# Kernel tuning notes

Hardware: AMD Instinct MI355X
Metric: run time of the kernel (lower is better)

The kernel has to match this reference:

```python
import jax, jax.numpy as jnp
import numpy as np

N_BALLS, BALL, DIM, HEADS = 16, 512, 256, 8
DH = DIM // HEADS            # 32
WIN = BALL // 16             # sliding window = 32
CBS = BALL // 16             # compress block size = 32
CST = BALL // 32             # compress stride = 16
FBS = BALL // 16             # fine (selection) block size = 32
NCB = (BALL - CBS) // CST + 1  # 31 compressed blocks
NFB = BALL // FBS              # 16 fine blocks
NB = BALL // WIN               # 16 sliding blocks
SCALE = DH ** -0.5

# ---- static index maps / masks (numpy, baked at trace time) ----
_qi = np.arange(BALL)
WIDX = np.arange(NCB)[:, None] * CST + np.arange(CBS)[None, :]          # (NCB, CBS)
_blk_end = np.arange(NCB) * CST + CBS - 1
CMASK = np.concatenate([np.ones((BALL, 1), bool), _qi[:, None] >= _blk_end[None, :]], axis=1)  # (m, NCB+1), col0 = mem kv
OVERLAP = np.zeros((NCB, NFB), np.float32)  # fraction of compressed block j overlapping fine block f
for _j in range(NCB):
    _a, _b = _j * CST, _j * CST + CBS
    for _f in range(NFB):
        _fa, _fb = _f * FBS, (_f + 1) * FBS
        OVERLAP[_j, _f] = max(0, min(_b, _fb) - max(_a, _fa)) / CBS
SELMASK = np.arange(NFB)[None, :] < (_qi // FBS)[:, None]   # only strictly-past fine blocks selectable
HAS_SEL = (_qi // FBS) > 0
OWN_TRI = (_qi % FBS)[:, None] >= np.arange(FBS)[None, :]   # causal mask inside own fine block
_qq = np.arange(WIN)[None, :, None]
_kk = np.arange(2 * WIN)[None, None, :]
_bb = np.arange(NB)[:, None, None]
SWMASK = (_kk > _qq) & (_kk <= _qq + WIN) & ((_bb > 0) | (_kk >= WIN))
NEG = -jnp.inf


def _rot(x, tpos):
    # interleaved rotary over full head dim; x: (n,H,m,DH)
    d2 = DH // 2
    inv = 1.0 / (10000.0 ** (jnp.arange(d2, dtype=jnp.float32) / d2))
    ang = tpos[:, None] * inv[None, :]
    cos, sin = jnp.cos(ang), jnp.sin(ang)
    x1, x2 = x[..., 0::2], x[..., 1::2]
    return jnp.stack((x1 * cos - x2 * sin, x1 * sin + x2 * cos), axis=-1).reshape(x.shape)


def _gmlp(xw, w1, w2):
    # per-head grouped MLP compressing each window: (n,H,NCB,CBS,DH) -> (n,H,NCB,DH)
    f = xw.reshape(xw.shape[0], HEADS, NCB, CBS * DH)
    h = jax.nn.relu(jnp.einsum('nhbi,hio->nhbo', f, w1))
    return jnp.einsum('nhbi,hio->nhbo', h, w2)


def _forward(x, pos, Wpe, bpe, rms_w, Wqkv, kpos, vpos, kw1, kw2, vw1, vw2, mem_ck, mem_cv, Wg, Wo):
    n, m = N_BALLS, BALL
    # relative position embedding w.r.t. ball center (eq. 9)
    pb = pos.reshape(n, m, -1)
    rel = pb - pb.mean(axis=1, keepdims=True)
    hx = x.reshape(n, m, DIM) + rel @ Wpe + bpe
    # RMSNorm
    hn = hx * jax.lax.rsqrt(jnp.mean(hx * hx, axis=-1, keepdims=True) + 1e-6) * rms_w
    q, k, v = jnp.split(hn @ Wqkv, 3, axis=-1)
    heads = lambda t: t.reshape(n, m, HEADS, DH).transpose(0, 2, 1, 3)
    q, k, v = heads(q), heads(k), heads(v)
    tpos = jnp.arange(m, dtype=jnp.float32)
    rq, rk = _rot(q, tpos), _rot(k, tpos)

    # ---- compressed branch (non-rotated q/k, intra-block pos emb, 1 learned mem kv) ----
    kw = k[:, :, WIDX] + kpos[None, :, None]        # (n,H,NCB,CBS,DH)
    vw = v[:, :, WIDX] + vpos[None, :, None]
    ck = _gmlp(kw, kw1, kw2)
    cv = _gmlp(vw, vw1, vw2)
    ckf = jnp.concatenate([jnp.broadcast_to(mem_ck[None], (n, HEADS, 1, DH)), ck], axis=2)
    cvf = jnp.concatenate([jnp.broadcast_to(mem_cv[None], (n, HEADS, 1, DH)), cv], axis=2)
    csim = jnp.einsum('nhid,nhjd->nhij', q, ckf) * SCALE
    cattn = jax.nn.softmax(jnp.where(CMASK[None, None], csim, NEG), axis=-1)
    c_out = jnp.einsum('nhij,nhjd->nhid', cattn, cvf)

    # ---- fine selection: importance from compressed attn probs -> top-1 past fine block ----
    imp = jnp.einsum('nhij,jf->nhif', cattn[..., 1:], jnp.asarray(OVERLAP))  # (n,H,m,NFB)
    sel = jnp.argmax(jnp.where(SELMASK[None, None], imp, NEG), axis=-1)     # (n,H,m)
    kb = rk.reshape(n, HEADS, NFB, FBS, DH)
    vb = v.reshape(n, HEADS, NFB, FBS, DH)
    qb = rq.reshape(n, HEADS, NFB, FBS, DH)
    own_s = (jnp.einsum('nhfqd,nhfkd->nhfqk', qb, kb) * SCALE).reshape(n, HEADS, m, FBS)
    fk = jnp.take_along_axis(kb, sel[..., None, None], axis=2)  # (n,H,m,FBS,DH) gather
    fv = jnp.take_along_axis(vb, sel[..., None, None], axis=2)
    sel_s = jnp.einsum('nhid,nhikd->nhik', rq, fk) * SCALE
    scores = jnp.concatenate([jnp.where(OWN_TRI[None, None], own_s, NEG),
                              jnp.where(HAS_SEL[None, None, :, None], sel_s, NEG)], axis=-1)
    fattn = jax.nn.softmax(scores, axis=-1)
    f_out = (jnp.einsum('nhfqk,nhfkd->nhfqd', fattn[..., :FBS].reshape(n, HEADS, NFB, FBS, FBS), vb).reshape(n, HEADS, m, DH)
             + jnp.einsum('nhik,nhikd->nhid', fattn[..., FBS:], fv))

    # ---- sliding window branch (causal local attention, look-back 1 block) ----
    qw = rq.reshape(n, HEADS, NB, WIN, DH)
    kwb = rk.reshape(n, HEADS, NB, WIN, DH)
    vwb = v.reshape(n, HEADS, NB, WIN, DH)
    pad = ((0, 0), (0, 0), (1, 0), (0, 0), (0, 0))
    K2 = jnp.concatenate([jnp.pad(kwb, pad)[:, :, :NB], kwb], axis=3)
    V2 = jnp.concatenate([jnp.pad(vwb, pad)[:, :, :NB], vwb], axis=3)
    s_sw = jnp.einsum('nhbqd,nhbkd->nhbqk', qw, K2) * SCALE
    sattn = jax.nn.softmax(jnp.where(SWMASK[None, None], s_sw, NEG), axis=-1)
    sw_out = jnp.einsum('nhbqk,nhbkd->nhbqd', sattn, V2).reshape(n, HEADS, m, DH)

    # ---- sigmoid-gated combine of the 3 strategies, merge heads, out proj ----
    gates = jax.nn.sigmoid(hn @ Wg).reshape(n, m, HEADS, 3).transpose(0, 2, 1, 3)  # (n,H,m,3)
    o = c_out * gates[..., 0:1] + f_out * gates[..., 1:2] + sw_out * gates[..., 2:3]
    o = o.transpose(0, 2, 1, 3).reshape(n, m, DIM)
    return (o @ Wo).reshape(n * m, DIM)


def setup_inputs() -> dict:
    key = jax.random.key(0)
    ks = jax.random.split(key, 16)
    s = 0.02
    N = N_BALLS * BALL
    return dict(
        x=jax.random.normal(ks[0], (N, DIM), jnp.float32),
        pos=jax.random.normal(ks[1], (N, 3), jnp.float32),
        Wpe=s * jax.random.normal(ks[2], (3, DIM), jnp.float32),
        bpe=jnp.zeros((DIM,), jnp.float32),
        rms_w=jnp.ones((DIM,), jnp.float32),
        Wqkv=s * jax.random.normal(ks[3], (DIM, 3 * DIM), jnp.float32),
        kpos=s * jax.random.normal(ks[4], (HEADS, CBS, DH), jnp.float32),
        vpos=s * jax.random.normal(ks[5], (HEADS, CBS, DH), jnp.float32),
        kw1=s * jax.random.normal(ks[6], (HEADS, CBS * DH, CBS * DH), jnp.float32),
        kw2=s * jax.random.normal(ks[7], (HEADS, CBS * DH, DH), jnp.float32),
        vw1=s * jax.random.normal(ks[8], (HEADS, CBS * DH, CBS * DH), jnp.float32),
        vw2=s * jax.random.normal(ks[9], (HEADS, CBS * DH, DH), jnp.float32),
        mem_ck=s * jax.random.normal(ks[10], (HEADS, 1, DH), jnp.float32),
        mem_cv=s * jax.random.normal(ks[11], (HEADS, 1, DH), jnp.float32),
        Wg=s * jax.random.normal(ks[12], (DIM, 3 * HEADS), jnp.float32),
        Wo=s * jax.random.normal(ks[13], (DIM, DIM), jnp.float32),
    )


def reference(x, pos, Wpe, bpe, rms_w, Wqkv, kpos, vpos, kw1, kw2, vw1, vw2, mem_ck, mem_cv, Wg, Wo):
    return _forward(x, pos, Wpe, bpe, rms_w, Wqkv, kpos, vpos, kw1, kw2, vw1, vw2, mem_ck, mem_cv, Wg, Wo)
```

## Files before the change

### kernel.cpp

```cpp
#include <hip/hip_runtime.h>
#include <hip/hip_bf16.h>
#include <math.h>

#define SCALE_ 0.17677669529663687f

__global__ __launch_bounds__(256) void d_rope(float* __restrict__ rope) {
  int i = blockIdx.x * 256 + threadIdx.x;
  int t = i >> 4, j = i & 15;
  float inv = powf(10000.f, -(float)j / 16.f);
  float ang = (float)t * inv;
  rope[2 * i]     = cosf(ang);
  rope[2 * i + 1] = sinf(ang);
}

__global__ __launch_bounds__(256) void k_pm(const float* __restrict__ pos,
                                            float* __restrict__ pm) {
  __shared__ float ps[1536];
  int ball = blockIdx.x;
  for (int i = threadIdx.x; i < 1536; i += 256) ps[i] = pos[(size_t)ball * 1536 + i];
  __syncthreads();
  if (threadIdx.x < 3) {
    int c = threadIdx.x;
    float s = 0.f;
    for (int t = 0; t < 512; ++t) s += ps[t * 3 + c];
    pm[ball * 3 + c] = s * (1.f / 512.f);
  }
}

__global__ __launch_bounds__(256) void k_hn(const float* __restrict__ x,
                                            const float* __restrict__ pos,
                                            const float* __restrict__ pm,
                                            const float* __restrict__ Wpe,
                                            const float* __restrict__ bpe,
                                            const float* __restrict__ rmsw,
                                            float* __restrict__ hn) {
  __shared__ float hx[32][257];
  __shared__ float rr[32][3];
  __shared__ float invs[32];
  int tb = blockIdx.x * 32;
  if (threadIdx.x < 96) {
    int tok = threadIdx.x / 3, c = threadIdx.x % 3;
    rr[tok][c] = pos[(size_t)(tb + tok) * 3 + c] - pm[((tb + tok) >> 9) * 3 + c];
  }
  __syncthreads();
  for (int i = threadIdx.x; i < 8192; i += 256) {
    int tok = i >> 8, d = i & 255;
    float h = x[(size_t)(tb + tok) * 256 + d] + rr[tok][0] * Wpe[d] + rr[tok][1] * Wpe[256 + d]
            + rr[tok][2] * Wpe[512 + d] + bpe[d];
    hx[tok][d] = h;
  }
  __syncthreads();
  if (threadIdx.x < 32) {
    int tok = threadIdx.x;
    float ss = 0.f;
    for (int d = 0; d < 256; ++d) { float h = hx[tok][d]; ss += h * h; }
    invs[tok] = 1.f / sqrtf(ss * (1.f / 256.f) + 1e-6f);
  }
  __syncthreads();
  for (int i = threadIdx.x; i < 8192; i += 256) {
    int tok = i >> 8, d = i & 255;
    hn[(size_t)(tb + tok) * 256 + d] = hx[tok][d] * invs[tok] * rmsw[d];
  }
}

__global__ __launch_bounds__(256) void k_qkv(const float* __restrict__ A,
                                             const float* __restrict__ B,
                                             const float* __restrict__ rope,
                                             float* __restrict__ qo,
                                             float* __restrict__ ko,
                                             float* __restrict__ vo,
                                             float* __restrict__ rqo,
                                             float* __restrict__ rko) {
  __shared__ float As[32][66];
  __shared__ __align__(16) float Bs[32][68];
  const int m0 = blockIdx.x * 64;
  const int n0 = blockIdx.y * 64;
  const int tid = threadIdx.x;
  const int tx = tid & 15, ty = tid >> 4;
  float acc[4][4] = {};
  for (int k0 = 0; k0 < 256; k0 += 32) {
#pragma unroll
    for (int i = 0; i < 8; ++i) {
      int li = tid + i * 256;
      int mm = li >> 5, c = li & 31;
      As[c][mm] = A[(size_t)(m0 + mm) * 256 + k0 + c];
    }
#pragma unroll
    for (int i = 0; i < 8; ++i) {
      int li = tid + i * 256;
      int r = li >> 6, c = li & 63;
      Bs[r][c] = B[(size_t)(k0 + r) * 768 + n0 + c];
    }
    __syncthreads();
#pragma unroll
    for (int kk = 0; kk < 32; ++kk) {
      float2 a0 = *reinterpret_cast<const float2*>(&As[kk][ty * 4]);
      float2 a1 = *reinterpret_cast<const float2*>(&As[kk][ty * 4 + 2]);
      float4 b4 = *reinterpret_cast<const float4*>(&Bs[kk][tx * 4]);
      float a[4] = {a0.x, a0.y, a1.x, a1.y};
      float b[4] = {b4.x, b4.y, b4.z, b4.w};
#pragma unroll
      for (int i = 0; i < 4; ++i)
#pragma unroll
        for (int j = 0; j < 4; ++j) acc[i][j] += a[i] * b[j];
    }
    __syncthreads();
  }
#pragma unroll
  for (int i = 0; i < 4; ++i) {
    int row = m0 + ty * 4 + i;
    int nb = row >> 9, t = row & 511;
#pragma unroll
    for (int j = 0; j < 4; j += 2) {
      int col = n0 + tx * 4 + j;
      int which = col >> 8, cj = col & 255;
      int h = cj >> 5, d = cj & 31;
      float v1 = acc[i][j], v2 = acc[i][j + 1];
      size_t base = ((size_t)(nb * 8 + h) * 512 + t) * 32 + d;
      if (which == 0) {
        qo[base] = v1; qo[base + 1] = v2;
        int p = d >> 1;
        float cc = rope[(t * 16 + p) * 2], ss = rope[(t * 16 + p) * 2 + 1];
        rqo[base] = v1 * cc - v2 * ss; rqo[base + 1] = v1 * ss + v2 * cc;
      } else if (which == 1) {
        ko[base] = v1; ko[base + 1] = v2;
        int p = d >> 1;
        float cc = rope[(t * 16 + p) * 2], ss = rope[(t * 16 + p) * 2 + 1];
        rko[base] = v1 * cc - v2 * ss; rko[base + 1] = v1 * ss + v2 * cc;
      } else {
        vo[base] = v1; vo[base + 1] = v2;
      }
    }
  }
}

__global__ __launch_bounds__(256) void d_gates(const float* __restrict__ hn,
                                               const float* __restrict__ Wg,
                                               float* __restrict__ gates) {
  int gid = blockIdx.x * 256 + threadIdx.x;
  int tok = gid / 24, j = gid % 24;
  const float* hr = hn + (size_t)tok * 256;
  float s = 0.f;
  for (int d = 0; d < 256; ++d) s += hr[d] * Wg[d * 24 + j];
  gates[gid] = 1.f / (1.f + expf(-s));
}

__global__ __launch_bounds__(256) void k_gmlp1(const float* __restrict__ kv,
                                               const float* __restrict__ posw,
                                               const float* __restrict__ w1,
                                               float* __restrict__ hb) {
  __shared__ float As[32][66];
  __shared__ __align__(16) float Bs[32][68];
  const int bid = blockIdx.x;
  const int xcd = bid & 7;
  const int idx = bid >> 3;
  const int mt  = idx & 7;
  const int nh  = xcd * 16 + (idx >> 3);
  const int n0 = (nh & 15) * 64;
  const int h  = nh >> 4;
  const int m0 = mt * 64;
  const int tid = threadIdx.x;
  const int tx = tid & 15, ty = tid >> 4;
  float acc[4][4] = {};
  for (int k0 = 0; k0 < 1024; k0 += 32) {
#pragma unroll
    for (int i = 0; i < 8; ++i) {
      int li = tid + i * 256;
      int mm = li >> 5, c = li & 31;
      int row = m0 + mm;
      float vv = 0.f;
      if (row < 496) {
        int nb = row / 31, bb = row % 31;
        vv = kv[((size_t)(nb * 8 + h) * 512 + bb * 16) * 32 + k0 + c] + posw[h * 1024 + k0 + c];
      }
      As[c][mm] = vv;
    }
#pragma unroll
    for (int i = 0; i < 8; ++i) {
      int li = tid + i * 256;
      int r = li >> 6, c = li & 63;
      Bs[r][c] = w1[(size_t)h * 1048576 + (size_t)(k0 + r) * 1024 + n0 + c];
    }
    __syncthreads();
#pragma unroll
    for (int kk = 0; kk < 32; ++kk) {
      float2 a0 = *reinterpret_cast<const float2*>(&As[kk][ty * 4]);
      float2 a1 = *reinterpret_cast<const float2*>(&As[kk][ty * 4 + 2]);
      float4 b4 = *reinterpret_cast<const float4*>(&Bs[kk][tx * 4]);
      float a[4] = {a0.x, a0.y, a1.x, a1.y};
      float b[4] = {b4.x, b4.y, b4.z, b4.w};
#pragma unroll
      for (int i = 0; i < 4; ++i)
#pragma unroll
        for (int j = 0; j < 4; ++j) acc[i][j] += a[i] * b[j];
    }
    __syncthreads();
  }
#pragma unroll
  for (int i = 0; i < 4; ++i) {
    int row = m0 + ty * 4 + i;
    if (row < 496) {
#pragma unroll
      for (int j = 0; j < 4; ++j)
        hb[((size_t)h * 496 + row) * 1024 + n0 + tx * 4 + j] = fmaxf(acc[i][j], 0.f);
    }
  }
}

__global__ __launch_bounds__(256) void d_g2(const float* __restrict__ hh,
                                            const float* __restrict__ w2,
                                            float* __restrict__ outp) {
  int gid = blockIdx.x * 256 + threadIdx.x;
  int o = gid & 31;
  int rem = gid >> 5;
  int h = rem / 496, row = rem % 496;
  int nb = row / 31, bb = row % 31;
  const float* hr = hh + (size_t)rem * 1024;
  const float* w2p = w2 + (size_t)h * 32768 + o;
  float s = 0.f;
  for (int i = 0; i < 1024; ++i) s += hr[i] * w2p[(size_t)i * 32];
  outp[((size_t)(nb * 8 + h) * 31 + bb) * 32 + o] = s;
}

__global__ __launch_bounds__(256) void d_cattn(const float* __restrict__ q,
                                               const float* __restrict__ ck,
                                               const float* __restrict__ cv,
                                               const float* __restrict__ mem_ck,
                                               const float* __restrict__ mem_cv,
                                               const float* __restrict__ gates,
                                               float* __restrict__ obuf,
                                               int* __restrict__ sel) {
  int gid = blockIdx.x * 256 + threadIdx.x;
  int nh = gid >> 9, t = gid & 511;
  int h = nh & 7, ball = nh >> 3;
  const float* qp = q + (size_t)gid * 32;
  float sc[32];
  float mx = -INFINITY;
#pragma unroll
  for (int j = 0; j < 32; ++j) {
    float s = -INFINITY;
    bool valid = (j == 0) || (t >= (j - 1) * 16 + 31);
    if (valid) {
      const float* kp = (j == 0) ? (mem_ck + h * 32)
                                 : (ck + ((size_t)nh * 31 + (j - 1)) * 32);
      s = 0.f;
      for (int d = 0; d < 32; ++d) s += qp[d] * kp[d];
      s *= SCALE_;
    }
    sc[j] = s;
    mx = fmaxf(mx, s);
  }
  float e[32];
  float den = 0.f;
#pragma unroll
  for (int j = 0; j < 32; ++j) { e[j] = expf(sc[j] - mx); den += e[j]; }
  float num[32];
#pragma unroll
  for (int d = 0; d < 32; ++d) num[d] = 0.f;
#pragma unroll
  for (int j = 0; j < 32; ++j) {
    const float* vp = (j == 0) ? (mem_cv + h * 32)
                               : (cv + ((size_t)nh * 31 + (j - 1)) * 32);
    float p = e[j];
    for (int d = 0; d < 32; ++d) num[d] += p * vp[d];
  }
  float inv = 1.f / den;
  float g0 = gates[(size_t)(ball * 512 + t) * 24 + h * 3];
  float* op = obuf + (size_t)(ball * 512 + t) * 256 + h * 32;
  for (int d = 0; d < 32; ++d) op[d] = num[d] * inv * g0;

  int s_idx = 0;
  if (t >= 32) {
    int fn = t >> 5;
    float best = -INFINITY;
    for (int f = 0; f < fn; ++f) {
      float im = 0.f;
#pragma unroll
      for (int j = 0; j < 31; ++j) {
        int a = j * 16, b2 = a + 32, fa = f * 32, fb = fa + 32;
        int lo = a > fa ? a : fa;
        int hi = b2 < fb ? b2 : fb;
        if (hi > lo) im += e[j + 1] * (float)(hi - lo) * (1.f / 32.f);
      }
      if (im > best) { best = im; s_idx = f; }
    }
  }
  sel[gid] = s_idx;
}

__global__ __launch_bounds__(256) void k_fattn(const float* __restrict__ rq,
                                               const float* __restrict__ rk,
                                               const float* __restrict__ v,
                                               const int* __restrict__ sel,
                                               const float* __restrict__ gates,
                                               float* __restrict__ obuf) {
  int f0 = blockIdx.x, h = blockIdx.y, nb = blockIdx.z;
  int nh = nb * 8 + h;
  __shared__ float rqs[32][33], rks[32][33], vs[32][33];
  for (int i = threadIdx.x; i < 1024; i += 256) {
    int r = i >> 5, d = i & 31;
    size_t base = ((size_t)nh * 512 + f0 * 32 + r) * 32 + d;
    rqs[r][d] = rq[base];
    rks[r][d] = rk[base];
    vs[r][d]  = v[base];
  }
  __syncthreads();
  int qi = threadIdx.x >> 3, l = threadIdx.x & 7;
  int t = f0 * 32 + qi;
  int sb = sel[(size_t)nh * 512 + t];
  bool hs = (t >= 32);
  float p[8];
  float mx = -INFINITY;
#pragma unroll
  for (int kk2 = 0; kk2 < 8; ++kk2) {
    int kk = l * 8 + kk2;
    float s = -INFINITY;
    if (kk < 32) {
      if (qi >= kk) {
        s = 0.f;
#pragma unroll
        for (int d = 0; d < 32; ++d) s += rqs[qi][d] * rks[kk][d];
        s *= SCALE_;
      }
    } else if (hs) {
      const float* kp = rk + ((size_t)nh * 512 + sb * 32 + (kk - 32)) * 32;
      s = 0.f;
#pragma unroll
      for (int d = 0; d < 32; ++d) s += rqs[qi][d] * kp[d];
      s *= SCALE_;
    }
    p[kk2] = s;
    mx = fmaxf(mx, s);
  }
#pragma unroll
  for (int off = 4; off; off >>= 1) mx = fmaxf(mx, __shfl_xor(mx, off, 8));
  float sum = 0.f;
#pragma unroll
  for (int kk2 = 0; kk2 < 8; ++kk2) { p[kk2] = expf(p[kk2] - mx); sum += p[kk2]; }
#pragma unroll
  for (int off = 4; off; off >>= 1) sum += __shfl_xor(sum, off, 8);
  float inv = 1.f / sum;
  float acc[32];
#pragma unroll
  for (int d = 0; d < 32; ++d) acc[d] = 0.f;
#pragma unroll
  for (int kk2 = 0; kk2 < 8; ++kk2) {
    int kk = l * 8 + kk2;
    float pw = p[kk2] * inv;
    if (kk < 32) {
#pragma unroll
      for (int d = 0; d < 32; ++d) acc[d] += pw * vs[kk][d];
    } else if (hs) {
      const float* vp = v + ((size_t)nh * 512 + sb * 32 + (kk - 32)) * 32;
#pragma unroll
      for (int d = 0; d < 32; ++d) acc[d] += pw * vp[d];
    }
  }
#pragma unroll
  for (int off = 4; off; off >>= 1) {
#pragma unroll
    for (int d = 0; d < 32; ++d) acc[d] += __shfl_xor(acc[d], off, 8);
  }
  float g1 = gates[(size_t)(nb * 512 + t) * 24 + h * 3 + 1];
  float* op = obuf + (size_t)(nb * 512 + t) * 256 + h * 32;
#pragma unroll
  for (int j = 0; j < 4; ++j) op[l * 4 + j] += acc[l * 4 + j] * g1;
}

__global__ __launch_bounds__(256) void k_swattn(const float* __restrict__ rq,
                                                const float* __restrict__ rk,
                                                const float* __restrict__ v,
                                                const float* __restrict__ gates,
                                                float* __restrict__ obuf) {
  int b = blockIdx.x, h = blockIdx.y, nb = blockIdx.z;
  int nh = nb * 8 + h;
  __shared__ float rqs[32][33], k2s[64][33], v2s[64][33];
  for (int i = threadIdx.x; i < 1024; i += 256) {
    int r = i >> 5, d = i & 31;
    rqs[r][d] = rq[((size_t)nh * 512 + b * 32 + r) * 32 + d];
  }
  for (int i = threadIdx.x; i < 2048; i += 256) {
    int r = i >> 5, d = i & 31;
    int tk = (b - 1) * 32 + r;
    float kk_ = 0.f, vv_ = 0.f;
    if (tk >= 0) {
      kk_ = rk[((size_t)nh * 512 + tk) * 32 + d];
      vv_ = v[((size_t)nh * 512 + tk) * 32 + d];
    }
    k2s[r][d] = kk_;
    v2s[r][d] = vv_;
  }
  __syncthreads();
  int qi = threadIdx.x >> 3, l = threadIdx.x & 7;
  int t = b * 32 + qi;
  float p[8];
  float mx = -INFINITY;
#pragma unroll
  for (int kk2 = 0; kk2 < 8; ++kk2) {
    int kk = l * 8 + kk2;
    bool valid = (kk > qi) && (kk <= qi + 32) && ((b > 0) || (kk >= 32));
    float s = -INFINITY;
    if (valid) {
      s = 0.f;
#pragma unroll
      for (int d = 0; d < 32; ++d) s += rqs[qi][d] * k2s[kk][d];
      s *= SCALE_;
    }
    p[kk2] = s;
    mx = fmaxf(mx, s);
  }
#pragma unroll
  for (int off = 4; off; off >>= 1) mx = fmaxf(mx, __shfl_xor(mx, off, 8));
  float sum = 0.f;
#pragma unroll
  for (int kk2 = 0; kk2 < 8; ++kk2) { p[kk2] = expf(p[kk2] - mx); sum += p[kk2]; }
#pragma unroll
  for (int off = 4; off; off >>= 1) sum += __shfl_xor(sum, off, 8);
  float inv = 1.f / sum;
  float acc[32];
#pragma unroll
  for (int d = 0; d < 32; ++d) acc[d] = 0.f;
#pragma unroll
  for (int kk2 = 0; kk2 < 8; ++kk2) {
    int kk = l * 8 + kk2;
    float pw = p[kk2] * inv;
#pragma unroll
    for (int d = 0; d < 32; ++d) acc[d] += pw * v2s[kk][d];
  }
#pragma unroll
  for (int off = 4; off; off >>= 1) {
#pragma unroll
    for (int d = 0; d < 32; ++d) acc[d] += __shfl_xor(acc[d], off, 8);
  }
  float g2 = gates[(size_t)(nb * 512 + t) * 24 + h * 3 + 2];
  float* op = obuf + (size_t)(nb * 512 + t) * 256 + h * 32;
#pragma unroll
  for (int j = 0; j < 4; ++j) op[l * 4 + j] += acc[l * 4 + j] * g2;
}

__global__ __launch_bounds__(256) void k_out(const float* __restrict__ A,
                                             const float* __restrict__ B,
                                             float* __restrict__ C) {
  __shared__ float As[32][66];
  __shared__ __align__(16) float Bs[32][68];
  const int m0 = blockIdx.x * 64;
  const int n0 = blockIdx.y * 64;
  const int tid = threadIdx.x;
  const int tx = tid & 15, ty = tid >> 4;
  float acc[4][4] = {};
  for (int k0 = 0; k0 < 256; k0 += 32) {
#pragma unroll
    for (int i = 0; i < 8; ++i) {
      int li = tid + i * 256;
      int mm = li >> 5, c = li & 31;
      As[c][mm] = A[(size_t)(m0 + mm) * 256 + k0 + c];
    }
#pragma unroll
    for (int i = 0; i < 8; ++i) {
      int li = tid + i * 256;
      int r = li >> 6, c = li & 63;
      Bs[r][c] = B[(size_t)(k0 + r) * 256 + n0 + c];
    }
    __syncthreads();
#pragma unroll
    for (int kk = 0; kk < 32; ++kk) {
      float2 a0 = *reinterpret_cast<const float2*>(&As[kk][ty * 4]);
      float2 a1 = *reinterpret_cast<const float2*>(&As[kk][ty * 4 + 2]);
      float4 b4 = *reinterpret_cast<const float4*>(&Bs[kk][tx * 4]);
      float a[4] = {a0.x, a0.y, a1.x, a1.y};
      float b[4] = {b4.x, b4.y, b4.z, b4.w};
#pragma unroll
      for (int i = 0; i < 4; ++i)
#pragma unroll
        for (int j = 0; j < 4; ++j) acc[i][j] += a[i] * b[j];
    }
    __syncthreads();
  }
#pragma unroll
  for (int i = 0; i < 4; ++i) {
    int row = m0 + ty * 4 + i;
#pragma unroll
    for (int j = 0; j < 4; ++j)
      C[(size_t)row * 256 + n0 + tx * 4 + j] = acc[i][j];
  }
}

extern "C" void kernel_launch(void* const* d_in, const int* in_sizes, int n_in,
                              void* d_out, int out_size, void* d_ws, size_t ws_size,
                              hipStream_t stream) {
  const float* x      = (const float*)d_in[0];
  const float* pos    = (const float*)d_in[1];
  const float* Wpe    = (const float*)d_in[2];
  const float* bpe    = (const float*)d_in[3];
  const float* rms_w  = (const float*)d_in[4];
  const float* Wqkv   = (const float*)d_in[5];
  const float* kpos   = (const float*)d_in[6];
  const float* vpos   = (const float*)d_in[7];
  const float* kw1    = (const float*)d_in[8];
  const float* kw2    = (const float*)d_in[9];
  const float* vw1    = (const float*)d_in[10];
  const float* vw2    = (const float*)d_in[11];
  const float* mem_ck = (const float*)d_in[12];
  const float* mem_cv = (const float*)d_in[13];
  const float* Wg     = (const float*)d_in[14];
  const float* Wo     = (const float*)d_in[15];
  float* out = (float*)d_out;

  float* ws = (float*)d_ws;
  const size_t TOK = 2097152;
  float* hn    = ws;
  float* q     = ws + TOK;
  float* k     = ws + 2 * TOK;
  float* v     = ws + 3 * TOK;
  float* rq    = ws + 4 * TOK;
  float* rk    = ws + 5 * TOK;
  float* obuf  = ws + 6 * TOK;
  float* hh    = ws + 7 * TOK;
  float* ck    = hh + 4063232;
  float* cv    = ck + 126976;
  float* gates = cv + 126976;
  float* rope  = gates + 196608;
  float* pm    = rope + 16384;
  int*   sel   = (int*)(pm + 64);

  d_rope<<<32, 256, 0, stream>>>(rope);
  k_pm<<<16, 256, 0, stream>>>(pos, pm);
  k_hn<<<256, 256, 0, stream>>>(x, pos, pm, Wpe, bpe, rms_w, hn);
  k_qkv<<<dim3(128, 12), 256, 0, stream>>>(hn, Wqkv, rope, q, k, v, rq, rk);
  d_gates<<<768, 256, 0, stream>>>(hn, Wg, gates);
  k_gmlp1<<<1024, 256, 0, stream>>>(k, kpos, kw1, hh);
  d_g2<<<496, 256, 0, stream>>>(hh, kw2, ck);
  k_gmlp1<<<1024, 256, 0, stream>>>(v, vpos, vw1, hh);
  d_g2<<<496, 256, 0, stream>>>(hh, vw2, cv);
  d_cattn<<<256, 256, 0, stream>>>(q, ck, cv, mem_ck, mem_cv, gates, obuf, sel);
  k_fattn<<<dim3(16, 8, 16), 256, 0, stream>>>(rq, rk, v, sel, gates, obuf);
  k_swattn<<<dim3(16, 8, 16), 256, 0, stream>>>(rq, rk, v, gates, obuf);
  k_out<<<dim3(128, 4), 256, 0, stream>>>(obuf, Wo, out);
}
```

Before: 611.7 us.

## Fuse gates into RMSnorm, stage compressed KV in LDS, swizzle GEMM blocks across XCDs

```diff
diff --git a/kernel.cpp b/kernel.cpp
--- a/kernel.cpp
+++ b/kernel.cpp
@@ -33,7 +33,9 @@
                                             const float* __restrict__ Wpe,
                                             const float* __restrict__ bpe,
                                             const float* __restrict__ rmsw,
-                                            float* __restrict__ hn) {
+                                            const float* __restrict__ Wg,
+                                            float* __restrict__ hn,
+                                            float* __restrict__ gates) {
   __shared__ float hx[32][257];
   __shared__ float rr[32][3];
   __shared__ float invs[32];
@@ -59,7 +61,16 @@
   __syncthreads();
   for (int i = threadIdx.x; i < 8192; i += 256) {
     int tok = i >> 8, d = i & 255;
-    hn[(size_t)(tb + tok) * 256 + d] = hx[tok][d] * invs[tok] * rmsw[d];
+    float hv = hx[tok][d] * invs[tok] * rmsw[d];
+    hn[(size_t)(tb + tok) * 256 + d] = hv;
+    hx[tok][d] = hv;
+  }
+  __syncthreads();
+  for (int g = threadIdx.x; g < 768; g += 256) {
+    int tok = g / 24, j = g % 24;
+    float s = 0.f;
+    for (int d = 0; d < 256; ++d) s += hx[tok][d] * Wg[d * 24 + j];
+    gates[(size_t)(tb + tok) * 24 + j] = 1.f / (1.f + expf(-s));
   }
 }
 
@@ -73,8 +84,11 @@
                                              float* __restrict__ rko) {
   __shared__ float As[32][66];
   __shared__ __align__(16) float Bs[32][68];
-  const int m0 = blockIdx.x * 64;
-  const int n0 = blockIdx.y * 64;
+  const int bid = blockIdx.x;
+  const int xcd = bid & 7;
+  const int idx = bid >> 3;
+  const int m0 = (xcd * 16 + (idx & 15)) * 64;
+  const int n0 = (idx >> 4) * 64;
   const int tid = threadIdx.x;
   const int tx = tid & 15, ty = tid >> 4;
   float acc[4][4] = {};
@@ -134,23 +148,13 @@
   }
 }
 
-__global__ __launch_bounds__(256) void d_gates(const float* __restrict__ hn,
-                                               const float* __restrict__ Wg,
-                                               float* __restrict__ gates) {
-  int gid = blockIdx.x * 256 + threadIdx.x;
-  int tok = gid / 24, j = gid % 24;
-  const float* hr = hn + (size_t)tok * 256;
-  float s = 0.f;
-  for (int d = 0; d < 256; ++d) s += hr[d] * Wg[d * 24 + j];
-  gates[gid] = 1.f / (1.f + expf(-s));
-}
-
 __global__ __launch_bounds__(256) void k_gmlp1(const float* __restrict__ kv,
                                                const float* __restrict__ posw,
                                                const float* __restrict__ w1,
                                                float* __restrict__ hb) {
   __shared__ float As[32][66];
   __shared__ __align__(16) float Bs[32][68];
+  __shared__ int rowbase[64];
   const int bid = blockIdx.x;
   const int xcd = bid & 7;
   const int idx = bid >> 3;
@@ -161,18 +165,24 @@
   const int m0 = mt * 64;
   const int tid = threadIdx.x;
   const int tx = tid & 15, ty = tid >> 4;
+  if (tid < 64) {
+    int row = m0 + tid;
+    if (row < 496) {
+      int nb = row / 31, bb = row % 31;
+      rowbase[tid] = ((nb * 8 + h) * 512 + bb * 16) * 32;
+    } else rowbase[tid] = -1;
+  }
+  __syncthreads();
   float acc[4][4] = {};
+  const float* pw = posw + h * 1024;
   for (int k0 = 0; k0 < 1024; k0 += 32) {
 #pragma unroll
     for (int i = 0; i < 8; ++i) {
       int li = tid + i * 256;
       int mm = li >> 5, c = li & 31;
-      int row = m0 + mm;
+      int base = rowbase[mm];
       float vv = 0.f;
-      if (row < 496) {
-        int nb = row / 31, bb = row % 31;
-        vv = kv[((size_t)(nb * 8 + h) * 512 + bb * 16) * 32 + k0 + c] + posw[h * 1024 + k0 + c];
-      }
+      if (base >= 0) vv = kv[(size_t)base + k0 + c] + pw[k0 + c];
       As[c][mm] = vv;
     }
 #pragma unroll
@@ -222,7 +232,7 @@
   outp[((size_t)(nb * 8 + h) * 31 + bb) * 32 + o] = s;
 }
 
-__global__ __launch_bounds__(256) void d_cattn(const float* __restrict__ q,
+__global__ __launch_bounds__(256) void k_cattn(const float* __restrict__ q,
                                                const float* __restrict__ ck,
                                                const float* __restrict__ cv,
                                                const float* __restrict__ mem_ck,
@@ -230,62 +240,69 @@
                                                const float* __restrict__ gates,
                                                float* __restrict__ obuf,
                                                int* __restrict__ sel) {
-  int gid = blockIdx.x * 256 + threadIdx.x;
-  int nh = gid >> 9, t = gid & 511;
+  int nh = blockIdx.x;
   int h = nh & 7, ball = nh >> 3;
-  const float* qp = q + (size_t)gid * 32;
-  float sc[32];
-  float mx = -INFINITY;
-#pragma unroll
-  for (int j = 0; j < 32; ++j) {
-    float s = -INFINITY;
-    bool valid = (j == 0) || (t >= (j - 1) * 16 + 31);
-    if (valid) {
-      const float* kp = (j == 0) ? (mem_ck + h * 32)
-                                 : (ck + ((size_t)nh * 31 + (j - 1)) * 32);
-      s = 0.f;
-      for (int d = 0; d < 32; ++d) s += qp[d] * kp[d];
-      s *= SCALE_;
-    }
-    sc[j] = s;
-    mx = fmaxf(mx, s);
-  }
-  float e[32];
-  float den = 0.f;
-#pragma unroll
-  for (int j = 0; j < 32; ++j) { e[j] = expf(sc[j] - mx); den += e[j]; }
-  float num[32];
-#pragma unroll
-  for (int d = 0; d < 32; ++d) num[d] = 0.f;
-#pragma unroll
-  for (int j = 0; j < 32; ++j) {
-    const float* vp = (j == 0) ? (mem_cv + h * 32)
-                               : (cv + ((size_t)nh * 31 + (j - 1)) * 32);
-    float p = e[j];
-    for (int d = 0; d < 32; ++d) num[d] += p * vp[d];
-  }
-  float inv = 1.f / den;
-  float g0 = gates[(size_t)(ball * 512 + t) * 24 + h * 3];
-  float* op = obuf + (size_t)(ball * 512 + t) * 256 + h * 32;
-  for (int d = 0; d < 32; ++d) op[d] = num[d] * inv * g0;
-
-  int s_idx = 0;
-  if (t >= 32) {
-    int fn = t >> 5;
-    float best = -INFINITY;
-    for (int f = 0; f < fn; ++f) {
-      float im = 0.f;
-#pragma unroll
-      for (int j = 0; j < 31; ++j) {
-        int a = j * 16, b2 = a + 32, fa = f * 32, fb = fa + 32;
-        int lo = a > fa ? a : fa;
-        int hi = b2 < fb ? b2 : fb;
-        if (hi > lo) im += e[j + 1] * (float)(hi - lo) * (1.f / 32.f);
+  __shared__ float kf[32][33], vf[32][33];
+  for (int i = threadIdx.x; i < 1024; i += 256) {
+    int j = i >> 5, d = i & 31;
+    kf[j][d] = (j == 0) ? mem_ck[h * 32 + d] : ck[((size_t)nh * 31 + j - 1) * 32 + d];
+    vf[j][d] = (j == 0) ? mem_cv[h * 32 + d] : cv[((size_t)nh * 31 + j - 1) * 32 + d];
+  }
+  __syncthreads();
+  for (int t = threadIdx.x; t < 512; t += 256) {
+    const float* qp = q + ((size_t)nh * 512 + t) * 32;
+    float qr[32];
+#pragma unroll
+    for (int d = 0; d < 32; ++d) qr[d] = qp[d];
+    float sc[32];
+    float mx = -INFINITY;
+#pragma unroll
+    for (int j = 0; j < 32; ++j) {
+      float s = -INFINITY;
+      bool valid = (j == 0) || (t >= (j - 1) * 16 + 31);
+      if (valid) {
+        s = 0.f;
+        for (int d = 0; d < 32; ++d) s += qr[d] * kf[j][d];
+        s *= SCALE_;
       }
-      if (im > best) { best = im; s_idx = f; }
-    }
-  }
-  sel[gid] = s_idx;
+      sc[j] = s;
+      mx = fmaxf(mx, s);
+    }
+    float e[32];
+    float den = 0.f;
+#pragma unroll
+    for (int j = 0; j < 32; ++j) { e[j] = expf(sc[j] - mx); den += e[j]; }
+    float num[32];
+#pragma unroll
+    for (int d = 0; d < 32; ++d) num[d] = 0.f;
+#pragma unroll
+    for (int j = 0; j < 32; ++j) {
+      float p = e[j];
+      for (int d = 0; d < 32; ++d) num[d] += p * vf[j][d];
+    }
+    float inv = 1.f / den;
+    float g0 = gates[(size_t)(ball * 512 + t) * 24 + h * 3];
+    float* op = obuf + (size_t)(ball * 512 + t) * 256 + h * 32;
+    for (int d = 0; d < 32; ++d) op[d] = num[d] * inv * g0;
+
+    int s_idx = 0;
+    if (t >= 32) {
+      int fn = t >> 5;
+      float best = -INFINITY;
+      for (int f = 0; f < fn; ++f) {
+        float im = 0.f;
+#pragma unroll
+        for (int j = 0; j < 31; ++j) {
+          int a = j * 16, b2 = a + 32, fa = f * 32, fb = fa + 32;
+          int lo = a > fa ? a : fa;
+          int hi = b2 < fb ? b2 : fb;
+          if (hi > lo) im += e[j + 1] * (float)(hi - lo) * (1.f / 32.f);
+        }
+        if (im > best) { best = im; s_idx = f; }
+      }
+    }
+    sel[(size_t)nh * 512 + t] = s_idx;
+  }
 }
 
 __global__ __launch_bounds__(256) void k_fattn(const float* __restrict__ rq,
@@ -443,8 +460,11 @@
                                              float* __restrict__ C) {
   __shared__ float As[32][66];
   __shared__ __align__(16) float Bs[32][68];
-  const int m0 = blockIdx.x * 64;
-  const int n0 = blockIdx.y * 64;
+  const int bid = blockIdx.x;
+  const int xcd = bid & 7;
+  const int idx = bid >> 3;
+  const int m0 = (xcd * 16 + (idx & 15)) * 64;
+  const int n0 = (idx >> 4) * 64;
   const int tid = threadIdx.x;
   const int tx = tid & 15, ty = tid >> 4;
   float acc[4][4] = {};
@@ -525,15 +545,14 @@
 
   d_rope<<<32, 256, 0, stream>>>(rope);
   k_pm<<<16, 256, 0, stream>>>(pos, pm);
-  k_hn<<<256, 256, 0, stream>>>(x, pos, pm, Wpe, bpe, rms_w, hn);
-  k_qkv<<<dim3(128, 12), 256, 0, stream>>>(hn, Wqkv, rope, q, k, v, rq, rk);
-  d_gates<<<768, 256, 0, stream>>>(hn, Wg, gates);
+  k_hn<<<256, 256, 0, stream>>>(x, pos, pm, Wpe, bpe, rms_w, Wg, hn, gates);
+  k_qkv<<<1536, 256, 0, stream>>>(hn, Wqkv, rope, q, k, v, rq, rk);
   k_gmlp1<<<1024, 256, 0, stream>>>(k, kpos, kw1, hh);
   d_g2<<<496, 256, 0, stream>>>(hh, kw2, ck);
   k_gmlp1<<<1024, 256, 0, stream>>>(v, vpos, vw1, hh);
   d_g2<<<496, 256, 0, stream>>>(hh, vw2, cv);
-  d_cattn<<<256, 256, 0, stream>>>(q, ck, cv, mem_ck, mem_cv, gates, obuf, sel);
+  k_cattn<<<128, 256, 0, stream>>>(q, ck, cv, mem_ck, mem_cv, gates, obuf, sel);
   k_fattn<<<dim3(16, 8, 16), 256, 0, stream>>>(rq, rk, v, sel, gates, obuf);
   k_swattn<<<dim3(16, 8, 16), 256, 0, stream>>>(rq, rk, v, gates, obuf);
-  k_out<<<dim3(128, 4), 256, 0, stream>>>(obuf, Wo, out);
-}
+  k_out<<<512, 256, 0, stream>>>(obuf, Wo, out);
+}
```

Measured after the change: 620.4 us. No clear change (+1.4%).
